# Kernel tuning notes

Hardware: AMD Instinct MI355X
Metric: run time of the kernel (lower is better)

The kernel has to match this reference:

```python
import jax, jax.numpy as jnp
import numpy as np

NUM_FRAMES = 36
NUM_QUERIES = 36000            # num_out = 1000
NUM_TGT = 256                  # flat targets = NUM_TGT * NUM_FRAMES = 9216
NUM_CLASSES = 81
COST_CLASS = 1.0
COST_BBOX = 1.0
COST_GIOU = 1.0


def box_cxcywh_to_xyxy(b):
    cx, cy, w, h = b[..., 0], b[..., 1], b[..., 2], b[..., 3]
    return jnp.stack([cx - 0.5 * w, cy - 0.5 * h, cx + 0.5 * w, cy + 0.5 * h], axis=-1)


def multi_giou(a, b):
    # elementwise (broadcasted) generalized IoU over last-dim xyxy boxes
    lt = jnp.maximum(a[..., :2], b[..., :2])
    rb = jnp.minimum(a[..., 2:], b[..., 2:])
    wh = jnp.clip(rb - lt, 0.0)
    inter = wh[..., 0] * wh[..., 1]
    area_a = (a[..., 2] - a[..., 0]) * (a[..., 3] - a[..., 1])
    area_b = (b[..., 2] - b[..., 0]) * (b[..., 3] - b[..., 1])
    union = area_a + area_b - inter
    iou = inter / union
    lt_c = jnp.minimum(a[..., :2], b[..., :2])
    rb_c = jnp.maximum(a[..., 2:], b[..., 2:])
    wh_c = jnp.clip(rb_c - lt_c, 0.0)
    area_c = wh_c[..., 0] * wh_c[..., 1]
    return iou - (area_c - union) / area_c


def setup_inputs() -> dict:
    key = jax.random.key(0)
    k1, k2, k3, k4 = jax.random.split(key, 4)
    pred_logits = jax.random.normal(k1, (NUM_QUERIES, NUM_CLASSES), dtype=jnp.float32)
    pred_boxes = jax.random.uniform(k2, (NUM_QUERIES, 4), dtype=jnp.float32,
                                    minval=0.05, maxval=0.95)
    tgt_bbox = jax.random.uniform(k3, (NUM_TGT * NUM_FRAMES, 4), dtype=jnp.float32,
                                  minval=0.05, maxval=0.95)
    tgt_ids = jax.random.randint(k4, (NUM_TGT * NUM_FRAMES,), 0, NUM_CLASSES)
    return {
        "pred_logits": pred_logits,
        "pred_boxes": pred_boxes,
        "tgt_bbox": tgt_bbox,
        "tgt_ids": tgt_ids,
        "num_frames": NUM_FRAMES,
    }


def reference(pred_logits, pred_boxes, tgt_bbox, tgt_ids, num_frames):
    Q, C = pred_logits.shape
    F = num_frames
    O = Q // F                      # num_out (queries per frame / tracks)
    T = tgt_ids.shape[0] // F       # num targets (tracks)

    out_prob = jax.nn.softmax(pred_logits, axis=-1)
    # [F, O, C] -> [O, F, C]
    out_prob_split = jnp.transpose(out_prob.reshape(F, O, C), (1, 0, 2))
    # gather over (frame, class) pairs: frame_index repeats 0..F-1 per target
    frame_index = jnp.tile(jnp.arange(F), T)          # [T*F]
    class_cost = -out_prob_split[:, frame_index, tgt_ids]      # [O, T*F]
    class_cost = class_cost.reshape(O, T, F).mean(axis=-1)     # [O, T]

    # [O, 1, F, 4] vs [1, T, F, 4]
    out_bbox_split = jnp.transpose(pred_boxes.reshape(F, O, 4), (1, 0, 2))[:, None]
    tgt_bbox_split = tgt_bbox.reshape(T, F, 4)[None]
    bbox_cost = jnp.abs(out_bbox_split - tgt_bbox_split).mean(axis=(-1, -2))  # [O, T]

    giou = multi_giou(box_cxcywh_to_xyxy(out_bbox_split),
                      box_cxcywh_to_xyxy(tgt_bbox_split))       # [O, T, F]
    iou_cost = -giou.mean(axis=-1)                              # [O, T]

    cost = COST_CLASS * class_cost + COST_BBOX * bbox_cost + COST_GIOU * iou_cost
    return cost
```

## Files before the change

kernel.cpp:

```cpp
#include <hip/hip_runtime.h>
#include <hip/hip_bf16.h>

#define NF 36
#define NO 1000
#define NT 256
#define NC 81

#define WS_FLOATS (NF * NT * 9)
#define WS_BYTES  (WS_FLOATS * 4)

__global__ __launch_bounds__(256) void matcher_prep_kernel(
    const float* __restrict__ tboxes,
    const int*   __restrict__ tids,
    float4* __restrict__ tb_c,
    float4* __restrict__ tb_x,
    int*    __restrict__ ids_t)
{
    const int i = blockIdx.x * 256 + threadIdx.x;
    if (i >= NF * NT) return;
    const int f = i / NT, t = i - f * NT;
    const float4 b = ((const float4*)tboxes)[t * NF + f];
    tb_c[i] = b;
    float4 x;
    x.x = b.x - 0.5f * b.z;  x.y = b.y - 0.5f * b.w;
    x.z = b.x + 0.5f * b.z;  x.w = b.y + 0.5f * b.w;
    tb_x[i] = x;
    ids_t[i] = tids[t * NF + f];
}

__global__ __launch_bounds__(256, 4) void matcher_main_kernel(
    const float* __restrict__ logits,
    const float* __restrict__ pboxes,
    const float4* __restrict__ tb_c,
    const float4* __restrict__ tb_x,
    const int*    __restrict__ ids_t,
    float* __restrict__ out)
{
    const int o    = blockIdx.x;
    const int tid  = threadIdx.x;
    const int wave = tid >> 6;
    const int lane = tid & 63;

    __shared__ float prob[NF * NC];

    for (int f = wave; f < NF; f += 4) {
        const float* row = logits + (size_t)(f * NO + o) * NC;
        float e1 = (lane      < NC) ? __expf(row[lane])      : 0.0f;
        float e2 = (lane + 64 < NC) ? __expf(row[lane + 64]) : 0.0f;
        float s = e1 + e2;
        #pragma unroll
        for (int m = 32; m; m >>= 1) s += __shfl_xor(s, m);
        const float inv = __builtin_amdgcn_rcpf(s);
        if (lane      < NC) prob[f * NC + lane]      = e1 * inv;
        if (lane + 64 < NC) prob[f * NC + lane + 64] = e2 * inv;
    }
    __syncthreads();

    const int t = tid;
    float acc_cls = 0.0f, acc_l1 = 0.0f, acc_giou = 0.0f;

    #pragma unroll 6
    for (int f = 0; f < NF; ++f) {
        const int    cls = ids_t[f * NT + t];
        const float4 tc  = tb_c[f * NT + t];
        const float4 tx  = tb_x[f * NT + t];
        const float4 pc  = ((const float4*)pboxes)[f * NO + o];

        acc_cls += prob[f * NC + cls];

        acc_l1 += fabsf(pc.x - tc.x) + fabsf(pc.y - tc.y)
                + fabsf(pc.z - tc.z) + fabsf(pc.w - tc.w);

        const float ax0 = pc.x - 0.5f * pc.z, ay0 = pc.y - 0.5f * pc.w;
        const float ax1 = pc.x + 0.5f * pc.z, ay1 = pc.y + 0.5f * pc.w;

        const float ltx = fmaxf(ax0, tx.x), lty = fmaxf(ay0, tx.y);
        const float rbx = fminf(ax1, tx.z), rby = fminf(ay1, tx.w);
        const float iw = fmaxf(rbx - ltx, 0.0f), ih = fmaxf(rby - lty, 0.0f);
        const float inter = iw * ih;

        const float area_a = pc.z * pc.w;
        const float area_b = (tx.z - tx.x) * (tx.w - tx.y);
        const float uni = area_a + area_b - inter;

        const float cx0 = fminf(ax0, tx.x), cy0 = fminf(ay0, tx.y);
        const float cx1 = fmaxf(ax1, tx.z), cy1 = fmaxf(ay1, tx.w);
        const float area_c = fmaxf(cx1 - cx0, 0.0f) * fmaxf(cy1 - cy0, 0.0f);

        const float r_uni = __builtin_amdgcn_rcpf(uni);
        const float r_c   = __builtin_amdgcn_rcpf(area_c);
        acc_giou += inter * r_uni - (area_c - uni) * r_c;
    }

    const float inv_f  = 1.0f / (float)NF;
    const float inv_4f = 1.0f / (float)(4 * NF);
    out[(size_t)o * NT + t] = -acc_cls * inv_f + acc_l1 * inv_4f - acc_giou * inv_f;
}

__global__ __launch_bounds__(256) void matcher_fallback_kernel(
    const float* __restrict__ logits, const float* __restrict__ pboxes,
    const float* __restrict__ tboxes, const int* __restrict__ tids,
    float* __restrict__ out)
{
    const int o = blockIdx.x, tid = threadIdx.x;
    const int wave = tid >> 6, lane = tid & 63;
    __shared__ float prob[NF * NC];
    __shared__ float pb[NF][4];
    for (int f = wave; f < NF; f += 4) {
        const float* row = logits + (size_t)(f * NO + o) * NC;
        float e1 = (lane < NC) ? __expf(row[lane]) : 0.0f;
        float e2 = (lane + 64 < NC) ? __expf(row[lane + 64]) : 0.0f;
        float s = e1 + e2;
        #pragma unroll
        for (int m = 32; m; m >>= 1) s += __shfl_xor(s, m);
        const float inv = 1.0f / s;
        if (lane < NC)      prob[f * NC + lane]      = e1 * inv;
        if (lane + 64 < NC) prob[f * NC + lane + 64] = e2 * inv;
    }
    if (tid < NF * 4) {
        const int f = tid >> 2, k = tid & 3;
        pb[f][k] = pboxes[(size_t)(f * NO + o) * 4 + k];
    }
    __syncthreads();
    const int t = tid;
    const float4* tb4 = (const float4*)tboxes;
    float acc_cls = 0.0f, acc_l1 = 0.0f, acc_giou = 0.0f;
    for (int f = 0; f < NF; ++f) {
        const int cls = tids[t * NF + f];
        const float4 tb = tb4[t * NF + f];
        acc_cls += prob[f * NC + cls];
        const float pcx = pb[f][0], pcy = pb[f][1], pw = pb[f][2], ph = pb[f][3];
        acc_l1 += fabsf(pcx - tb.x) + fabsf(pcy - tb.y) + fabsf(pw - tb.z) + fabsf(ph - tb.w);
        const float ax0 = pcx - 0.5f * pw, ay0 = pcy - 0.5f * ph;
        const float ax1 = pcx + 0.5f * pw, ay1 = pcy + 0.5f * ph;
        const float bx0 = tb.x - 0.5f * tb.z, by0 = tb.y - 0.5f * tb.w;
        const float bx1 = tb.x + 0.5f * tb.z, by1 = tb.y + 0.5f * tb.w;
        const float ltx = fmaxf(ax0, bx0), lty = fmaxf(ay0, by0);
        const float rbx = fminf(ax1, bx1), rby = fminf(ay1, by1);
        const float inter = fmaxf(rbx - ltx, 0.0f) * fmaxf(rby - lty, 0.0f);
        const float uni = (ax1 - ax0) * (ay1 - ay0) + (bx1 - bx0) * (by1 - by0) - inter;
        const float cx0 = fminf(ax0, bx0), cy0 = fminf(ay0, by0);
        const float cx1 = fmaxf(ax1, bx1), cy1 = fmaxf(ay1, by1);
        const float area_c = fmaxf(cx1 - cx0, 0.0f) * fmaxf(cy1 - cy0, 0.0f);
        acc_giou += inter / uni - (area_c - uni) / area_c;
    }
    out[(size_t)o * NT + t] = (-acc_cls - acc_giou) * (1.0f / NF) + acc_l1 * (1.0f / (4 * NF));
}

extern "C" void kernel_launch(void* const* d_in, const int* in_sizes, int n_in,
                              void* d_out, int out_size, void* d_ws, size_t ws_size,
                              hipStream_t stream) {
    const float* pred_logits = (const float*)d_in[0];
    const float* pred_boxes  = (const float*)d_in[1];
    const float* tgt_bbox    = (const float*)d_in[2];
    const int*   tgt_ids     = (const int*)d_in[3];
    float* out = (float*)d_out;

    if (ws_size >= (size_t)WS_BYTES) {
        float4* tb_c  = (float4*)d_ws;
        float4* tb_x  = tb_c + NF * NT;
        int*    ids_t = (int*)(tb_x + NF * NT);
        matcher_prep_kernel<<<(NF * NT + 255) / 256, 256, 0, stream>>>(
            tgt_bbox, tgt_ids, tb_c, tb_x, ids_t);
        matcher_main_kernel<<<NO, 256, 0, stream>>>(
            pred_logits, pred_boxes, tb_c, tb_x, ids_t, out);
    } else {
        matcher_fallback_kernel<<<NO, 256, 0, stream>>>(
            pred_logits, pred_boxes, tgt_bbox, tgt_ids, out);
    }
}
```

Baseline: 90.11 us.

## Pack target ids to bytes, drop center boxes, precompute pred xyxy in LDS

Target classes are packed four per uchar4, and the cxcywh target copy is dropped. The L1 term is now computed from xyxy corners through an algebraic identity, which cuts per-frame global loads from three streams to roughly one float4 plus a quarter of an id. Predicted boxes are converted to xyxy with their areas once per block in shared memory, so the inner loop does less arithmetic. The clamp on area_c is removed, and byte packing assumes class ids stay below 256.

Result: no change. 90.11 us (+0.0%).

```diff
diff --git a/kernel.cpp b/kernel.cpp
--- a/kernel.cpp
+++ b/kernel.cpp
@@ -6,34 +6,38 @@
 #define NT 256
 #define NC 81
 
-#define WS_FLOATS (NF * NT * 9)
-#define WS_BYTES  (WS_FLOATS * 4)
+#define WS_BYTES (NF * NT * 16 + (NF / 4) * NT * 4)
 
 __global__ __launch_bounds__(256) void matcher_prep_kernel(
     const float* __restrict__ tboxes,
     const int*   __restrict__ tids,
-    float4* __restrict__ tb_c,
     float4* __restrict__ tb_x,
-    int*    __restrict__ ids_t)
+    uchar4* __restrict__ pk)
 {
     const int i = blockIdx.x * 256 + threadIdx.x;
-    if (i >= NF * NT) return;
-    const int f = i / NT, t = i - f * NT;
-    const float4 b = ((const float4*)tboxes)[t * NF + f];
-    tb_c[i] = b;
-    float4 x;
-    x.x = b.x - 0.5f * b.z;  x.y = b.y - 0.5f * b.w;
-    x.z = b.x + 0.5f * b.z;  x.w = b.y + 0.5f * b.w;
-    tb_x[i] = x;
-    ids_t[i] = tids[t * NF + f];
+    if (i < NF * NT) {
+        const int f = i / NT, t = i - f * NT;
+        const float4 b = ((const float4*)tboxes)[t * NF + f];
+        float4 x;
+        x.x = b.x - 0.5f * b.z;  x.y = b.y - 0.5f * b.w;
+        x.z = b.x + 0.5f * b.z;  x.w = b.y + 0.5f * b.w;
+        tb_x[i] = x;
+    }
+    if (i < (NF / 4) * NT) {
+        const int fb4 = i / NT, t = i - fb4 * NT;
+        const int4 v = *(const int4*)(tids + t * NF + fb4 * 4);
+        uchar4 u;
+        u.x = (unsigned char)v.x;  u.y = (unsigned char)v.y;
+        u.z = (unsigned char)v.z;  u.w = (unsigned char)v.w;
+        pk[i] = u;
+    }
 }
 
 __global__ __launch_bounds__(256, 4) void matcher_main_kernel(
     const float* __restrict__ logits,
     const float* __restrict__ pboxes,
-    const float4* __restrict__ tb_c,
     const float4* __restrict__ tb_x,
-    const int*    __restrict__ ids_t,
+    const uchar4* __restrict__ pk,
     float* __restrict__ out)
 {
     const int o    = blockIdx.x;
@@ -41,7 +45,18 @@
     const int wave = tid >> 6;
     const int lane = tid & 63;
 
-    __shared__ float prob[NF * NC];
+    __shared__ float  prob[NF * NC];
+    __shared__ float4 pbx[NF];
+    __shared__ float  pbarea[NF];
+
+    if (tid < NF) {
+        const float4 pc = ((const float4*)pboxes)[tid * NO + o];
+        float4 x;
+        x.x = pc.x - 0.5f * pc.z;  x.y = pc.y - 0.5f * pc.w;
+        x.z = pc.x + 0.5f * pc.z;  x.w = pc.y + 0.5f * pc.w;
+        pbx[tid] = x;
+        pbarea[tid] = pc.z * pc.w;
+    }
 
     for (int f = wave; f < NF; f += 4) {
         const float* row = logits + (size_t)(f * NO + o) * NC;
@@ -59,37 +74,41 @@
     const int t = tid;
     float acc_cls = 0.0f, acc_l1 = 0.0f, acc_giou = 0.0f;
 
-    #pragma unroll 6
-    for (int f = 0; f < NF; ++f) {
-        const int    cls = ids_t[f * NT + t];
-        const float4 tc  = tb_c[f * NT + t];
-        const float4 tx  = tb_x[f * NT + t];
-        const float4 pc  = ((const float4*)pboxes)[f * NO + o];
+    #pragma unroll 2
+    for (int fb = 0; fb < NF; fb += 4) {
+        const uchar4 c4 = pk[(fb >> 2) * NT + t];
+        float4 tx[4];
+        #pragma unroll
+        for (int j = 0; j < 4; ++j) tx[j] = tb_x[(fb + j) * NT + t];
+        const int cls[4] = {c4.x, c4.y, c4.z, c4.w};
 
-        acc_cls += prob[f * NC + cls];
+        #pragma unroll
+        for (int j = 0; j < 4; ++j) {
+            const int f = fb + j;
+            const float4 tv = tx[j];
+            const float4 pb = pbx[f];
 
-        acc_l1 += fabsf(pc.x - tc.x) + fabsf(pc.y - tc.y)
-                + fabsf(pc.z - tc.z) + fabsf(pc.w - tc.w);
+            acc_cls += prob[f * NC + cls[j]];
 
-        const float ax0 = pc.x - 0.5f * pc.z, ay0 = pc.y - 0.5f * pc.w;
-        const float ax1 = pc.x + 0.5f * pc.z, ay1 = pc.y + 0.5f * pc.w;
+            const float dx0 = pb.x - tv.x, dy0 = pb.y - tv.y;
+            const float dx1 = pb.z - tv.z, dy1 = pb.w - tv.w;
+            acc_l1 += 0.5f * (fabsf(dx0 + dx1) + fabsf(dy0 + dy1))
+                    + fabsf(dx1 - dx0) + fabsf(dy1 - dy0);
 
-        const float ltx = fmaxf(ax0, tx.x), lty = fmaxf(ay0, tx.y);
-        const float rbx = fminf(ax1, tx.z), rby = fminf(ay1, tx.w);
-        const float iw = fmaxf(rbx - ltx, 0.0f), ih = fmaxf(rby - lty, 0.0f);
-        const float inter = iw * ih;
+            const float ltx = fmaxf(pb.x, tv.x), lty = fmaxf(pb.y, tv.y);
+            const float rbx = fminf(pb.z, tv.z), rby = fminf(pb.w, tv.w);
+            const float inter = fmaxf(rbx - ltx, 0.0f) * fmaxf(rby - lty, 0.0f);
 
-        const float area_a = pc.z * pc.w;
-        const float area_b = (tx.z - tx.x) * (tx.w - tx.y);
-        const float uni = area_a + area_b - inter;
+            const float area_b = (tv.z - tv.x) * (tv.w - tv.y);
+            const float uni = pbarea[f] + area_b - inter;
 
-        const float cx0 = fminf(ax0, tx.x), cy0 = fminf(ay0, tx.y);
-        const float cx1 = fmaxf(ax1, tx.z), cy1 = fmaxf(ay1, tx.w);
-        const float area_c = fmaxf(cx1 - cx0, 0.0f) * fmaxf(cy1 - cy0, 0.0f);
+            const float cx0 = fminf(pb.x, tv.x), cy0 = fminf(pb.y, tv.y);
+            const float cx1 = fmaxf(pb.z, tv.z), cy1 = fmaxf(pb.w, tv.w);
+            const float area_c = (cx1 - cx0) * (cy1 - cy0);
 
-        const float r_uni = __builtin_amdgcn_rcpf(uni);
-        const float r_c   = __builtin_amdgcn_rcpf(area_c);
-        acc_giou += inter * r_uni - (area_c - uni) * r_c;
+            acc_giou += inter * __builtin_amdgcn_rcpf(uni)
+                      - (area_c - uni) * __builtin_amdgcn_rcpf(area_c);
+        }
     }
 
     const float inv_f  = 1.0f / (float)NF;
@@ -157,13 +176,12 @@
     float* out = (float*)d_out;
 
     if (ws_size >= (size_t)WS_BYTES) {
-        float4* tb_c  = (float4*)d_ws;
-        float4* tb_x  = tb_c + NF * NT;
-        int*    ids_t = (int*)(tb_x + NF * NT);
+        float4* tb_x = (float4*)d_ws;
+        uchar4* pk   = (uchar4*)(tb_x + NF * NT);
         matcher_prep_kernel<<<(NF * NT + 255) / 256, 256, 0, stream>>>(
-            tgt_bbox, tgt_ids, tb_c, tb_x, ids_t);
+            tgt_bbox, tgt_ids, tb_x, pk);
         matcher_main_kernel<<<NO, 256, 0, stream>>>(
-            pred_logits, pred_boxes, tb_c, tb_x, ids_t, out);
+            pred_logits, pred_boxes, tb_x, pk, out);
     } else {
         matcher_fallback_kernel<<<NO, 256, 0, stream>>>(
             pred_logits, pred_boxes, tgt_bbox, tgt_ids, out);
```
